# Optimization experiments

Hardware: AMD Instinct MI355X
Metric: run time of the kernel (lower is better)

Reference implementation:

```python
import jax, jax.numpy as jnp
import numpy as np

N, D, H, K, P = 1536, 1024, 16, 64, 8
FREQ_DIM = 14 * 3 * 128  # freq_embedding(pos, 128) flattened


def freq_embedding(t, size):
    # min_freq=0.01, max_freq=2**8 as in the block's call sites
    nf = size // 2
    freqs = (2.0 ** jnp.linspace(np.log2(0.01), np.log2(256.0), nf)).astype(jnp.float32)
    r = t[..., None] * freqs
    return jnp.stack((jnp.sin(r), jnp.cos(r)), axis=-1).reshape(t.shape[0], -1)


def layer_norm(x, eps=1e-5):
    m = jnp.mean(x, -1, keepdims=True)
    v = jnp.var(x, -1, keepdims=True)
    return (x - m) * jax.lax.rsqrt(v + eps)


def cond_norm(x, cond, ws, bs, wb, bb):
    return jax.nn.sigmoid(cond @ ws + bs) * layer_norm(x) + (cond @ wb + bb)


def _unit(v):
    return v * jax.lax.rsqrt(jnp.sum(v * v, -1, keepdims=True) + 1e-8)


def aa_frames(pos):
    # Gram-Schmidt frame from backbone N/CA/C (atom14 slots 0,1,2)
    n, ca, c = pos[:, 0], pos[:, 1], pos[:, 2]
    e1 = _unit(c - ca)
    v2 = n - ca
    e2 = _unit(v2 - jnp.sum(e1 * v2, -1, keepdims=True) * e1)
    e3 = jnp.cross(e1, e2)
    R = jnp.stack([e1, e2, e3], axis=-1)  # [N,3,3]
    return R, ca


def setup_inputs():
    key = jax.random.key(0)
    ks = iter(jax.random.split(key, 64))
    r = lambda *s: jax.random.normal(next(ks), s, jnp.float32)
    w = lambda *s: 0.02 * jax.random.normal(next(ks), s, jnp.float32)
    z = lambda *s: jnp.zeros(s, jnp.float32)
    return dict(
        local=r(N, D), pos=r(N, 14, 3), condition=r(N, D),
        mask=jnp.ones((N,), bool), pair_bias=r(H, N, N),
        w_f1=w(FREQ_DIM, 2 * D), b_f1=z(2 * D), w_f2=w(2 * D, D), b_f2=z(D),
        cn1_ws=w(D, D), cn1_bs=z(D), cn1_wb=w(D, D), cn1_bb=z(D),
        wq=w(D, H * K), wk=w(D, H * K), wv=w(D, H * K),
        wqp=w(D, H * P * 3), wkp=w(D, H * P * 3), wvp=w(D, H * P * 3),
        gamma=z(H), wo=w(H * (K + 4 * P), D), bo=z(D),
        cn2_ws=w(D, D), cn2_bs=z(D), cn2_wb=w(D, D), cn2_bb=z(D),
        wg1=w(D, 2 * D), bg1=z(2 * D), wg2=w(D, 2 * D), bg2=z(2 * D),
        wg3=w(2 * D, D), bg3=z(D),
        cn3_ws=w(D, D), cn3_bs=z(D), cn3_wb=w(D, D), cn3_bb=z(D),
        w_vel=w(D, 14 * 3),
    )


def reference(local, pos, condition, mask, pair_bias,
              w_f1, b_f1, w_f2, b_f2,
              cn1_ws, cn1_bs, cn1_wb, cn1_bb,
              wq, wk, wv, wqp, wkp, wvp, gamma, wo, bo,
              cn2_ws, cn2_bs, cn2_wb, cn2_bb,
              wg1, bg1, wg2, bg2, wg3, bg3,
              cn3_ws, cn3_bs, cn3_wb, cn3_bb, w_vel):
    n = local.shape[0]
    # embed_pred_pos: MLP over freq embedding of coords
    emb = freq_embedding(pos, 128)  # [N, 5376]
    local = local + (jax.nn.silu(emb @ w_f1 + b_f1) @ w_f2 + b_f2)
    # attention branch
    ai = cond_norm(local, condition, cn1_ws, cn1_bs, cn1_wb, cn1_bb)
    R, t = aa_frames(pos)
    q = (ai @ wq).reshape(n, H, K)
    k = (ai @ wk).reshape(n, H, K)
    v = (ai @ wv).reshape(n, H, K)
    to_glob = lambda p: jnp.einsum('nab,nhpb->nhpa', R, p) + t[:, None, None, :]
    qg = to_glob((ai @ wqp).reshape(n, H, P, 3))
    kg = to_glob((ai @ wkp).reshape(n, H, P, 3))
    vg = to_glob((ai @ wvp).reshape(n, H, P, 3))
    qk = jnp.einsum('ihk,jhk->hij', q, k) / np.sqrt(K).astype(np.float32)
    # squared point distances via norm expansion (never materialize [H,N,N,P,3])
    ptdot = jnp.einsum('ihpc,jhpc->hij', qg, kg)
    qn = jnp.sum(qg * qg, axis=(-1, -2)).T  # [H,N]
    kn = jnp.sum(kg * kg, axis=(-1, -2)).T
    dist2 = qn[:, :, None] + kn[None if False else slice(None), None, :] - 2.0 * ptdot
    wc = np.sqrt(2.0 / (9.0 * P)).astype(np.float32)
    logits = qk + pair_bias - 0.5 * wc * jax.nn.softplus(gamma)[:, None, None] * dist2
    logits = jnp.where(mask[None, None, :], logits, -1e9)
    a = jax.nn.softmax(logits, axis=-1)  # [H,N,N]
    o = jnp.einsum('hij,jhk->ihk', a, v).reshape(n, H * K)
    opg = jnp.einsum('hij,jhpc->ihpc', a, vg)
    opl = jnp.einsum('nba,nhpb->nhpa', R, opg - t[:, None, None, :])
    onorm = jnp.sqrt(jnp.sum(opl * opl, -1) + 1e-8).reshape(n, -1)
    upd = jnp.concatenate([o, opl.reshape(n, -1), onorm], axis=-1) @ wo + bo
    local = local + upd
    # gated MLP branch
    x = cond_norm(local, condition, cn2_ws, cn2_bs, cn2_wb, cn2_bb)
    local = local + (jax.nn.silu(x @ wg1 + bg1) * (x @ wg2 + bg2)) @ wg3 + bg3
    # output heads
    ln = cond_norm(local, condition, cn3_ws, cn3_bs, cn3_wb, cn3_bb)
    velocity = (ln @ w_vel).reshape(n, 14, 3)
    return local, velocity
```

## Files before the change

kernel.cpp:

```cpp
#include <hip/hip_runtime.h>
#include <hip/hip_bf16.h>
#include <math.h>

#define NRES 1536
#define NH 16
#define NNF 2359296ull
#define LOG2E 1.44269504f
#define KVS 4
#define LDQ 4224
#define NTPJ 19
#define PROBLK 16914

typedef unsigned short u16;
typedef __attribute__((ext_vector_type(8))) short short8;
typedef __attribute__((ext_vector_type(4))) unsigned short u16x4;
typedef __attribute__((ext_vector_type(4))) float f32x4;

typedef const __attribute__((address_space(1))) void gvoid;
typedef __attribute__((address_space(3))) void lvoid;

__device__ __forceinline__ u16 f2b(float x){
    __hip_bfloat16 h = __float2bfloat16(x);
    return *reinterpret_cast<u16*>(&h);
}
__device__ __forceinline__ float b2f(u16 u){
    unsigned v = ((unsigned)u) << 16;
    return __uint_as_float(v);
}

#define F_BIAS  1
#define F_SILU  2
#define F_RESID 8
#define F_OUTBF 16

template<int TNF>
__global__ __launch_bounds__(256) void gemm_t(
    const u16* __restrict__ A, int lda, size_t zsA,
    const u16* __restrict__ BT, int ldb, size_t zsB,
    float* __restrict__ Cf, u16* __restrict__ Cb, int ldc, size_t zsC,
    const float* __restrict__ bias, size_t zsBias,
    const float* __restrict__ resid, int ldr, size_t zsR,
    int Ncols, int Kd, int flags, int ksl)
{
    constexpr int TN = TNF * 32;
    __shared__ u16 As[2][128 * 64];
    __shared__ u16 Bs[2][TN * 64];

    unsigned gx = gridDim.x, gy = gridDim.y;
    unsigned nb = gx * gy * gridDim.z;
    unsigned bid = (blockIdx.z * gy + blockIdx.y) * gx + blockIdx.x;
    if ((nb & 7u) == 0u) bid = (bid & 7u) * (nb >> 3) + (bid >> 3);
    const int bxi = bid % gx;
    const int byi = (bid / gx) % gy;
    const int bz  = bid / (gx * gy);

    const int tid = threadIdx.x;
    const int l = tid & 63, w = tid >> 6;
    const int bm = byi * 128, bn = bxi * TN;

    A  += zsA * bz;
    BT += zsB * bz;

    const int kbeg = ksl ? bz * ksl : 0;
    const int kend = ksl ? kbeg + ksl : Kd;
    const int nk = (kend - kbeg) >> 6;

    const int arow   = l >> 3;
    const int aslot  = l & 7;
    const int srcslt = aslot ^ arow;

    const u16* aBase[4];
    const u16* bBase[TN / 32];
    #pragma unroll
    for (int t = 0; t < 4; ++t) {
        int ra = bm + (w * 4 + t) * 8 + arow;
        aBase[t] = A + (size_t)ra * lda + srcslt * 8;
    }
    #pragma unroll
    for (int t = 0; t < TN / 32; ++t) {
        int rb = bn + (w * (TN / 32) + t) * 8 + arow;
        if (rb > Ncols - 1) rb = Ncols - 1;
        bBase[t] = BT + (size_t)rb * ldb + srcslt * 8;
    }

    const int wr = w >> 1, wc = w & 1;
    const int fr = l & 15;
    const int fq = l >> 4;

    f32x4 acc[4][TNF];
    #pragma unroll
    for (int i = 0; i < 4; ++i)
        #pragma unroll
        for (int j = 0; j < TNF; ++j) acc[i][j] = (f32x4){0.f, 0.f, 0.f, 0.f};

    auto stage = [&](int buf, int k0) {
        #pragma unroll
        for (int t = 0; t < 4; ++t)
            __builtin_amdgcn_global_load_lds((gvoid*)(aBase[t] + k0),
                (lvoid*)((char*)As[buf] + (w * 4 + t) * 1024), 16, 0, 0);
        #pragma unroll
        for (int t = 0; t < TN / 32; ++t)
            __builtin_amdgcn_global_load_lds((gvoid*)(bBase[t] + k0),
                (lvoid*)((char*)Bs[buf] + (w * (TN / 32) + t) * 1024), 16, 0, 0);
    };

    stage(0, kbeg);
    __syncthreads();
    int cur = 0;

    for (int it = 0; it < nk; ++it) {
        if (it + 1 < nk) stage(cur ^ 1, kbeg + (it + 1) * 64);
        #pragma unroll
        for (int kk = 0; kk < 2; ++kk) {
            const int slotR = ((kk * 4) + fq) ^ (l & 7);
            short8 av[4], bv[TNF];
            #pragma unroll
            for (int m = 0; m < 4; ++m) {
                int r = wr * 64 + m * 16 + fr;
                av[m] = *(const short8*)((const char*)As[cur] + r * 128 + slotR * 16);
            }
            #pragma unroll
            for (int n = 0; n < TNF; ++n) {
                int r = wc * (TNF * 16) + n * 16 + fr;
                bv[n] = *(const short8*)((const char*)Bs[cur] + r * 128 + slotR * 16);
            }
            #pragma unroll
            for (int m = 0; m < 4; ++m)
                #pragma unroll
                for (int n = 0; n < TNF; ++n)
                    acc[m][n] = __builtin_amdgcn_mfma_f32_16x16x32_bf16(av[m], bv[n], acc[m][n], 0, 0, 0);
        }
        __syncthreads();
        cur ^= 1;
    }

    const float* residz = (flags & F_RESID) ? resid + zsR * bz : nullptr;
    const float* biasz  = (flags & F_BIAS)  ? bias + zsBias * bz : nullptr;
    float* cfz = Cf ? Cf + zsC * bz : nullptr;
    u16*   cbz = Cb ? Cb + zsC * bz : nullptr;

    #pragma unroll
    for (int m = 0; m < 4; ++m) {
        #pragma unroll
        for (int n = 0; n < TNF; ++n) {
            int gc = bn + wc * (TNF * 16) + n * 16 + fr;
            if (gc >= Ncols) continue;
            int gr0 = bm + wr * 64 + m * 16 + fq * 4;
            #pragma unroll
            for (int r = 0; r < 4; ++r) {
                int gr = gr0 + r;
                float v = acc[m][n][r];
                if (flags & F_BIAS)  v += biasz[gc];
                if (flags & F_SILU)  v = v / (1.f + expf(-v));
                if (flags & F_RESID) v += residz[(size_t)gr * ldr + gc];
                if (flags & F_OUTBF) cbz[(size_t)gr * ldc + gc] = f2b(v);
                else                 cfz[(size_t)gr * ldc + gc] = v;
            }
        }
    }
}

struct GJob {
    const u16* A;
    const u16* BT;
    u16* C;
    const float* bias;
    int lda, ldb, ldc;
    size_t zsA, zsB, zsC, zsBias;
    int Nc, Kd, ksl, flags;
    unsigned gx, gy, start, nb;
};

__global__ __launch_bounds__(256) void gemm_dual(GJob j0, GJob j1)
{
    __shared__ u16 As[2][128 * 64];
    __shared__ u16 Bs[2][64 * 64];

    GJob J = (blockIdx.x >= j1.start) ? j1 : j0;
    unsigned bid = blockIdx.x - J.start;
    if ((J.nb & 7u) == 0u) bid = (bid & 7u) * (J.nb >> 3) + (bid >> 3);
    const int bxi = bid % J.gx;
    const int byi = (bid / J.gx) % J.gy;
    const int bz  = bid / (J.gx * J.gy);

    const int tid = threadIdx.x;
    const int l = tid & 63, w = tid >> 6;
    const int bm = byi * 128, bn = bxi * 64;

    const u16* A  = J.A + J.zsA * bz;
    const u16* BT = J.BT + J.zsB * bz;

    const int kbeg = J.ksl ? bz * J.ksl : 0;
    const int kend = J.ksl ? kbeg + J.ksl : J.Kd;
    const int nk = (kend - kbeg) >> 6;

    const int arow   = l >> 3;
    const int aslot  = l & 7;
    const int srcslt = aslot ^ arow;

    const u16* aBase[4];
    const u16* bBase[2];
    #pragma unroll
    for (int t = 0; t < 4; ++t) {
        int ra = bm + (w * 4 + t) * 8 + arow;
        aBase[t] = A + (size_t)ra * J.lda + srcslt * 8;
    }
    #pragma unroll
    for (int t = 0; t < 2; ++t) {
        int rb = bn + (w * 2 + t) * 8 + arow;
        if (rb > J.Nc - 1) rb = J.Nc - 1;
        bBase[t] = BT + (size_t)rb * J.ldb + srcslt * 8;
    }

    const int wr = w >> 1, wc = w & 1;
    const int fr = l & 15;
    const int fq = l >> 4;

    f32x4 acc[4][2];
    #pragma unroll
    for (int i = 0; i < 4; ++i)
        #pragma unroll
        for (int j = 0; j < 2; ++j) acc[i][j] = (f32x4){0.f, 0.f, 0.f, 0.f};

    auto stage = [&](int buf, int k0) {
        #pragma unroll
        for (int t = 0; t < 4; ++t)
            __builtin_amdgcn_global_load_lds((gvoid*)(aBase[t] + k0),
                (lvoid*)((char*)As[buf] + (w * 4 + t) * 1024), 16, 0, 0);
        #pragma unroll
        for (int t = 0; t < 2; ++t)
            __builtin_amdgcn_global_load_lds((gvoid*)(bBase[t] + k0),
                (lvoid*)((char*)Bs[buf] + (w * 2 + t) * 1024), 16, 0, 0);
    };

    stage(0, kbeg);
    __syncthreads();
    int cur = 0;

    for (int it = 0; it < nk; ++it) {
        if (it + 1 < nk) stage(cur ^ 1, kbeg + (it + 1) * 64);
        #pragma unroll
        for (int kk = 0; kk < 2; ++kk) {
            const int slotR = ((kk * 4) + fq) ^ (l & 7);
            short8 av[4], bv[2];
            #pragma unroll
            for (int m = 0; m < 4; ++m) {
                int r = wr * 64 + m * 16 + fr;
                av[m] = *(const short8*)((const char*)As[cur] + r * 128 + slotR * 16);
            }
            #pragma unroll
            for (int n = 0; n < 2; ++n) {
                int r = wc * 32 + n * 16 + fr;
                bv[n] = *(const short8*)((const char*)Bs[cur] + r * 128 + slotR * 16);
            }
            #pragma unroll
            for (int m = 0; m < 4; ++m)
                #pragma unroll
                for (int n = 0; n < 2; ++n)
                    acc[m][n] = __builtin_amdgcn_mfma_f32_16x16x32_bf16(av[m], bv[n], acc[m][n], 0, 0, 0);
        }
        __syncthreads();
        cur ^= 1;
    }

    const float* biasz = (J.flags & F_BIAS) ? J.bias + J.zsBias * bz : nullptr;
    u16* cbz = J.C + J.zsC * bz;

    #pragma unroll
    for (int m = 0; m < 4; ++m) {
        #pragma unroll
        for (int n = 0; n < 2; ++n) {
            int gc = bn + wc * 32 + n * 16 + fr;
            if (gc >= J.Nc) continue;
            int gr0 = bm + wr * 64 + m * 16 + fq * 4;
            #pragma unroll
            for (int r = 0; r < 4; ++r) {
                int gr = gr0 + r;
                float v = acc[m][n][r];
                if (J.flags & F_BIAS) v += biasz[gc];
                cbz[(size_t)gr * J.ldc + gc] = f2b(v);
            }
        }
    }
}

__global__ __launch_bounds__(256) void reduce_epi(
    const u16* __restrict__ part, size_t slice, int nsl,
    float* __restrict__ Cf, u16* __restrict__ Cb,
    const float* __restrict__ bias,
    const float* __restrict__ resid, int ldr,
    int M, int Ncols, int flags)
{
    if ((Ncols & 7) == 0) {
        size_t total8 = (size_t)M * Ncols / 8;
        for (size_t i8 = (size_t)blockIdx.x * 256 + threadIdx.x; i8 < total8;
             i8 += (size_t)gridDim.x * 256) {
            size_t i0 = i8 * 8;
            int r = (int)(i0 / (unsigned)Ncols);
            int c0 = (int)(i0 - (size_t)r * Ncols);
            float v[8] = {0,0,0,0,0,0,0,0};
            for (int s = 0; s < nsl; ++s) {
                const u16x4* p = (const u16x4*)(part + (size_t)s * slice + i0);
                u16x4 a = p[0], b = p[1];
                v[0] += b2f(a.x); v[1] += b2f(a.y); v[2] += b2f(a.z); v[3] += b2f(a.w);
                v[4] += b2f(b.x); v[5] += b2f(b.y); v[6] += b2f(b.z); v[7] += b2f(b.w);
            }
            #pragma unroll
            for (int j = 0; j < 8; ++j) {
                if (flags & F_BIAS) v[j] += bias[c0 + j];
                if (flags & F_SILU) v[j] = v[j] / (1.f + expf(-v[j]));
            }
            if (flags & F_RESID) {
                const float4* rp = (const float4*)(resid + (size_t)r * ldr + c0);
                float4 r0 = rp[0], r1 = rp[1];
                v[0] += r0.x; v[1] += r0.y; v[2] += r0.z; v[3] += r0.w;
                v[4] += r1.x; v[5] += r1.y; v[6] += r1.z; v[7] += r1.w;
            }
            if (flags & F_OUTBF) {
                short8 o;
                #pragma unroll
                for (int j = 0; j < 8; ++j) o[j] = (short)f2b(v[j]);
                *(short8*)(Cb + i0) = o;
            } else {
                float4 o0 = {v[0], v[1], v[2], v[3]}, o1 = {v[4], v[5], v[6], v[7]};
                float4* cp = (float4*)(Cf + i0);
                cp[0] = o0; cp[1] = o1;
            }
        }
    } else {
        size_t total = (size_t)M * Ncols;
        for (size_t i = (size_t)blockIdx.x * 256 + threadIdx.x; i < total;
             i += (size_t)gridDim.x * 256) {
            float v = 0.f;
            for (int s = 0; s < nsl; ++s) v += b2f(part[(size_t)s * slice + i]);
            if (flags & F_OUTBF) Cb[i] = f2b(v);
            else                 Cf[i] = v;
        }
    }
}

__global__ __launch_bounds__(256) void reduce_cn(
    const u16* __restrict__ part, size_t slice, int nsl,
    const float* __restrict__ bias, const float* __restrict__ resid,
    float* __restrict__ locOut,
    const u16* __restrict__ cs, const u16* __restrict__ cb,
    u16* __restrict__ normB)
{
    int row = blockIdx.x, tid = threadIdx.x;
    size_t base = (size_t)row * 1024 + tid * 4;
    float v[4];
    {
        float4 rv = *(const float4*)(resid + base);
        v[0] = rv.x; v[1] = rv.y; v[2] = rv.z; v[3] = rv.w;
    }
    for (int s = 0; s < nsl; ++s) {
        u16x4 p = *(const u16x4*)(part + (size_t)s * slice + base);
        v[0] += b2f(p.x); v[1] += b2f(p.y); v[2] += b2f(p.z); v[3] += b2f(p.w);
    }
    {
        float4 bv = *(const float4*)(bias + tid * 4);
        v[0] += bv.x; v[1] += bv.y; v[2] += bv.z; v[3] += bv.w;
    }
    *(float4*)(locOut + base) = (float4){v[0], v[1], v[2], v[3]};

    float s1 = v[0] + v[1] + v[2] + v[3];
    float s2 = v[0]*v[0] + v[1]*v[1] + v[2]*v[2] + v[3]*v[3];
    __shared__ float r1[256], r2[256];
    r1[tid] = s1; r2[tid] = s2;
    __syncthreads();
    for (int st = 128; st > 0; st >>= 1) {
        if (tid < st) { r1[tid] += r1[tid + st]; r2[tid] += r2[tid + st]; }
        __syncthreads();
    }
    float mean = r1[0] * (1.f / 1024.f);
    float var = r2[0] * (1.f / 1024.f) - mean * mean;
    float rs = rsqrtf(var + 1e-5f);
    u16x4 sv = *(const u16x4*)(cs + base);
    u16x4 bv = *(const u16x4*)(cb + base);
    u16x4 o;
    o.x = f2b((1.f / (1.f + expf(-b2f(sv.x)))) * (v[0] - mean) * rs + b2f(bv.x));
    o.y = f2b((1.f / (1.f + expf(-b2f(sv.y)))) * (v[1] - mean) * rs + b2f(bv.y));
    o.z = f2b((1.f / (1.f + expf(-b2f(sv.z)))) * (v[2] - mean) * rs + b2f(bv.z));
    o.w = f2b((1.f / (1.f + expf(-b2f(sv.w)))) * (v[3] - mean) * rs + b2f(bv.w));
    *(u16x4*)(normB + base) = o;
}

__global__ __launch_bounds__(256, 2) void attn_kernel(
    const u16* __restrict__ qe, const u16* __restrict__ ke,
    const u16* __restrict__ vt, const float* __restrict__ pb,
    u16* __restrict__ Opart, float* __restrict__ mlpart)
{
    __shared__ u16 Ks[2][64 * 128];
    __shared__ u16 Vs[2][96 * 64];
    __shared__ u16 Ps[64 * 64];

    unsigned gx = gridDim.x, gy = gridDim.y;
    unsigned nb = gx * gy * gridDim.z;
    unsigned bid = (blockIdx.z * gy + blockIdx.y) * gx + blockIdx.x;
    bid = (bid & 7u) * (nb >> 3) + (bid >> 3);
    const int qx = bid % gx;
    const int h  = (bid / gx) % gy;
    const int z  = bid / (gx * gy);

    const int tid = threadIdx.x;
    const int l = tid & 63, w = tid >> 6;
    const int q0 = qx * 64;
    const int fr = l & 15, fq = l >> 4;

    const u16* keh = ke + (size_t)h * NRES * 128;
    const u16* vth = vt + (size_t)h * 96 * NRES;

    const int kr4 = l >> 4, ks16 = l & 15;
    const int vr8 = l >> 3, vs8 = l & 7;

    short8 qv[4];
    {
        const u16* qrow = qe + ((size_t)h * NRES + (q0 + w * 16 + fr)) * 128 + fq * 8;
        #pragma unroll
        for (int kk = 0; kk < 4; ++kk)
            qv[kk] = *(const short8*)(qrow + kk * 32);
    }

    float m_run[4], l_run[4];
    f32x4 oacc[6];
    #pragma unroll
    for (int r = 0; r < 4; ++r) { m_run[r] = -1e30f; l_run[r] = 0.f; }
    #pragma unroll
    for (int n = 0; n < 6; ++n) oacc[n] = (f32x4){0.f, 0.f, 0.f, 0.f};

    const int NIT = NRES / 64 / KVS;
    const int jbase = z * (NRES / KVS);
    int cur = 0;

    auto stage = [&](int buf, int j0) {
        #pragma unroll
        for (int t = 0; t < 4; ++t) {
            int row = w * 16 + t * 4 + kr4;
            int ss = ks16 ^ (row & 7);
            __builtin_amdgcn_global_load_lds(
                (gvoid*)(keh + (size_t)(j0 + row) * 128 + ss * 8),
                (lvoid*)((char*)Ks[buf] + (w * 16 + t * 4) * 256), 16, 0, 0);
        }
        #pragma unroll
        for (int t = 0; t < 3; ++t) {
            int row = w * 24 + t * 8 + vr8;
            int ss = vs8 ^ (row & 7);
            __builtin_amdgcn_global_load_lds(
                (gvoid*)(vth + (size_t)row * NRES + j0 + ss * 8),
                (lvoid*)((char*)Vs[buf] + (w * 24 + t * 8) * 128), 16, 0, 0);
        }
    };
    const float* pbrow = pb + ((size_t)h * NRES + (q0 + w * 16 + fq * 4)) * NRES + fr;

    f32x4 pbv[4], pbn[4] = {};
    stage(0, jbase);
    #pragma unroll
    for (int n = 0; n < 4; ++n)
        #pragma unroll
        for (int r = 0; r < 4; ++r)
            pbv[n][r] = pbrow[(size_t)r * NRES + jbase + n * 16];
    __syncthreads();

    for (int it = 0; it < NIT; ++it) {
        if (it + 1 < NIT) {
            int j1 = jbase + (it + 1) * 64;
            stage(cur ^ 1, j1);
            #pragma unroll
            for (int n = 0; n < 4; ++n)
                #pragma unroll
                for (int r = 0; r < 4; ++r)
                    pbn[n][r] = pbrow[(size_t)r * NRES + j1 + n * 16];
        }

        f32x4 sacc[4];
        #pragma unroll
        for (int n = 0; n < 4; ++n) sacc[n] = (f32x4){0.f, 0.f, 0.f, 0.f};
        __builtin_amdgcn_s_setprio(1);
        #pragma unroll
        for (int kk = 0; kk < 4; ++kk) {
            #pragma unroll
            for (int n = 0; n < 4; ++n) {
                int row = n * 16 + fr;
                short8 bv = *(const short8*)((const char*)Ks[cur] + row * 256
                                             + (((kk * 4 + fq) ^ (fr & 7)) * 16));
                sacc[n] = __builtin_amdgcn_mfma_f32_16x16x32_bf16(qv[kk], bv, sacc[n], 0, 0, 0);
            }
        }
        __builtin_amdgcn_s_setprio(0);
        #pragma unroll
        for (int n = 0; n < 4; ++n) sacc[n] += pbv[n];

        float alpha[4];
        #pragma unroll
        for (int r = 0; r < 4; ++r) {
            float v = fmaxf(fmaxf(sacc[0][r], sacc[1][r]), fmaxf(sacc[2][r], sacc[3][r]));
            v = fmaxf(v, __shfl_xor(v, 1, 64));
            v = fmaxf(v, __shfl_xor(v, 2, 64));
            v = fmaxf(v, __shfl_xor(v, 4, 64));
            v = fmaxf(v, __shfl_xor(v, 8, 64));
            float mn = fmaxf(m_run[r], v);
            alpha[r] = exp2f((m_run[r] - mn) * LOG2E);
            m_run[r] = mn;
        }

        float psum[4] = {0.f, 0.f, 0.f, 0.f};
        #pragma unroll
        for (int n = 0; n < 4; ++n) {
            int col = n * 16 + fr;
            #pragma unroll
            for (int r = 0; r < 4; ++r) {
                float p = exp2f((sacc[n][r] - m_run[r]) * LOG2E);
                psum[r] += p;
                int rowf = w * 16 + fq * 4 + r;
                int byte = rowf * 128 + (((col >> 3) ^ (rowf & 7)) * 16) + (col & 7) * 2;
                *(u16*)((char*)Ps + byte) = f2b(p);
            }
        }
        #pragma unroll
        for (int r = 0; r < 4; ++r) {
            float v = psum[r];
            v += __shfl_xor(v, 1, 64);
            v += __shfl_xor(v, 2, 64);
            v += __shfl_xor(v, 4, 64);
            v += __shfl_xor(v, 8, 64);
            l_run[r] = l_run[r] * alpha[r] + v;
        }
        #pragma unroll
        for (int n = 0; n < 6; ++n)
            #pragma unroll
            for (int r = 0; r < 4; ++r)
                oacc[n][r] *= alpha[r];

        __builtin_amdgcn_s_setprio(1);
        #pragma unroll
        for (int kk = 0; kk < 2; ++kk) {
            int prow = w * 16 + fr;
            short8 pa = *(const short8*)((const char*)Ps + prow * 128
                                         + (((kk * 4 + fq) ^ (prow & 7)) * 16));
            #pragma unroll
            for (int n = 0; n < 6; ++n) {
                int vrow = n * 16 + fr;
                short8 vv = *(const short8*)((const char*)Vs[cur] + vrow * 128
                                             + (((kk * 4 + fq) ^ (fr & 7)) * 16));
                oacc[n] = __builtin_amdgcn_mfma_f32_16x16x32_bf16(pa, vv, oacc[n], 0, 0, 0);
            }
        }
        __builtin_amdgcn_s_setprio(0);

        __syncthreads();
        cur ^= 1;
        #pragma unroll
        for (int n = 0; n < 4; ++n) pbv[n] = pbn[n];
    }

    u16* Oz = Opart + ((size_t)z * NH + h) * NRES * 96;
    #pragma unroll
    for (int n = 0; n < 6; ++n) {
        int c = n * 16 + fr;
        #pragma unroll
        for (int r = 0; r < 4; ++r) {
            int row = q0 + w * 16 + fq * 4 + r;
            Oz[(size_t)row * 96 + c] = f2b(oacc[n][r]);
        }
    }
    if (fr == 0) {
        float* mlz = mlpart + ((size_t)z * NH + h) * NRES * 2;
        #pragma unroll
        for (int r = 0; r < 4; ++r) {
            int row = q0 + w * 16 + fq * 4 + r;
            mlz[row * 2 + 0] = m_run[r];
            mlz[row * 2 + 1] = l_run[r];
        }
    }
}

__global__ __launch_bounds__(256) void combine_fin(
    const u16* __restrict__ Opart, const float* __restrict__ mlpart,
    const float* __restrict__ Rb, const float* __restrict__ tb,
    u16* __restrict__ featB)
{
    int idx = blockIdx.x * 256 + threadIdx.x;
    if (idx >= NRES * NH) return;
    int n = idx >> 4, h = idx & 15;

    float m[KVS], lv[KVS], wgt[KVS];
    float mm = -1e30f;
    #pragma unroll
    for (int s = 0; s < KVS; ++s) {
        size_t rr = ((size_t)s * NH + h) * NRES + n;
        m[s] = mlpart[rr * 2];
        lv[s] = mlpart[rr * 2 + 1];
        mm = fmaxf(mm, m[s]);
    }
    float ll = 0.f;
    #pragma unroll
    for (int s = 0; s < KVS; ++s) {
        wgt[s] = exp2f((m[s] - mm) * LOG2E);
        ll += lv[s] * wgt[s];
    }
    float inv = 1.f / ll;
    const u16* op[KVS];
    #pragma unroll
    for (int s = 0; s < KVS; ++s)
        op[s] = Opart + (((size_t)s * NH + h) * NRES + n) * 96;

    u16* fb = featB + (size_t)n * 1536;
    #pragma unroll
    for (int k = 0; k < 64; ++k) {
        float v = 0.f;
        #pragma unroll
        for (int s = 0; s < KVS; ++s) v += b2f(op[s][k]) * wgt[s];
        fb[h * 64 + k] = f2b(v * inv);
    }

    float R[9];
    #pragma unroll
    for (int a = 0; a < 9; ++a) R[a] = Rb[(size_t)n * 9 + a];
    float t0 = tb[(size_t)n * 3 + 0], t1 = tb[(size_t)n * 3 + 1], t2 = tb[(size_t)n * 3 + 2];
    #pragma unroll
    for (int p = 0; p < 8; ++p) {
        float d[3];
        #pragma unroll
        for (int dd = 0; dd < 3; ++dd) {
            int c = 64 + p * 3 + dd;
            float v = 0.f;
            #pragma unroll
            for (int s = 0; s < KVS; ++s) v += b2f(op[s][c]) * wgt[s];
            d[dd] = v * inv;
        }
        float x = d[0] - t0, y = d[1] - t1, z = d[2] - t2;
        float a0 = R[0] * x + R[3] * y + R[6] * z;
        float a1 = R[1] * x + R[4] * y + R[7] * z;
        float a2 = R[2] * x + R[5] * y + R[8] * z;
        fb[1024 + h * 24 + p * 3 + 0] = f2b(a0);
        fb[1024 + h * 24 + p * 3 + 1] = f2b(a1);
        fb[1024 + h * 24 + p * 3 + 2] = f2b(a2);
        fb[1408 + h * 8 + p] = f2b(sqrtf(a0 * a0 + a1 * a1 + a2 * a2 + 1e-8f));
    }
}

struct TpMega {
    const float* src[NTPJ];
    u16* dst[NTPJ];
    int ldi[NTPJ], ldo[NTPJ], K[NTPJ], N[NTPJ];
    int bx[NTPJ], start[NTPJ];
};

__global__ __launch_bounds__(256) void prep_kernel(
    const float* __restrict__ pos, const float* __restrict__ cond,
    const float* __restrict__ cn1_bs, const float* __restrict__ cn1_bb,
    const float* __restrict__ cn2_bs, const float* __restrict__ cn2_bb,
    const float* __restrict__ cn3_bs, const float* __restrict__ cn3_bb,
    const float* __restrict__ bg1, const float* __restrict__ bg2,
    float* __restrict__ Rb, float* __restrict__ tb,
    u16* __restrict__ emb, u16* __restrict__ condB,
    float* __restrict__ bias2, float* __restrict__ biasg,
    TpMega J)
{
    __shared__ float t[32][33];
    int b = blockIdx.x, tid = threadIdx.x;
    if (b >= PROBLK) {
        int tb2 = b - PROBLK;
        int j = NTPJ - 1;
        while (J.start[j] > tb2) --j;
        int lb = tb2 - J.start[j];
        int bxn = J.bx[j];
        int n0 = (lb % bxn) * 32;
        int k0 = (lb / bxn) * 32;
        const float* in = J.src[j];
        u16* out = J.dst[j];
        int ldi = J.ldi[j], ldo = J.ldo[j], Kk = J.K[j], Nn = J.N[j];
        int tx = tid & 31, ty = tid >> 5;
        #pragma unroll
        for (int jj = 0; jj < 4; ++jj) {
            int k = k0 + ty + jj * 8;
            if (k < Kk && n0 + tx < Nn) t[ty + jj * 8][tx] = in[(size_t)k * ldi + n0 + tx];
        }
        __syncthreads();
        #pragma unroll
        for (int jj = 0; jj < 4; ++jj) {
            int n = n0 + ty + jj * 8;
            int k = k0 + tx;
            if (n < Nn && k < Kk) out[(size_t)n * ldo + k] = f2b(t[tx][ty + jj * 8]);
        }
        return;
    }
    if (b < 16128) {
        int idx = b * 256 + tid;
        int f = idx & 63;
        int rest = idx >> 6;
        int coord = rest % 42;
        int n = rest / 42;
        float tt = pos[(size_t)n * 42 + coord];
        const double l0 = -6.643856189774724;
        const double step = 14.643856189774724 / 63.0;
        float freq = exp2f((float)(l0 + f * step));
        float r = tt * freq;
        size_t o = (size_t)n * 5376 + (size_t)coord * 128 + 2 * f;
        emb[o]     = f2b(sinf(r));
        emb[o + 1] = f2b(cosf(r));
    } else if (b < 16896) {
        int i = (b - 16128) * 256 + tid;
        size_t i0 = (size_t)i * 8;
        const float4* p = (const float4*)(cond + i0);
        float4 a = p[0], bb = p[1];
        short8 o;
        o[0]=(short)f2b(a.x); o[1]=(short)f2b(a.y); o[2]=(short)f2b(a.z); o[3]=(short)f2b(a.w);
        o[4]=(short)f2b(bb.x); o[5]=(short)f2b(bb.y); o[6]=(short)f2b(bb.z); o[7]=(short)f2b(bb.w);
        *(short8*)(condB + i0) = o;
    } else if (b < 16902) {
        int n = (b - 16896) * 256 + tid;
        if (n >= NRES) return;
        const float* p = pos + (size_t)n * 42;
        float nx = p[0], ny = p[1], nz = p[2];
        float cax = p[3], cay = p[4], caz = p[5];
        float cx = p[6], cy = p[7], cz = p[8];
        float v1x = cx - cax, v1y = cy - cay, v1z = cz - caz;
        float i1 = rsqrtf(v1x * v1x + v1y * v1y + v1z * v1z + 1e-8f);
        float e1x = v1x * i1, e1y = v1y * i1, e1z = v1z * i1;
        float v2x = nx - cax, v2y = ny - cay, v2z = nz - caz;
        float d = e1x * v2x + e1y * v2y + e1z * v2z;
        float wx = v2x - d * e1x, wy = v2y - d * e1y, wz = v2z - d * e1z;
        float i2 = rsqrtf(wx * wx + wy * wy + wz * wz + 1e-8f);
        float e2x = wx * i2, e2y = wy * i2, e2z = wz * i2;
        float e3x = e1y * e2z - e1z * e2y;
        float e3y = e1z * e2x - e1x * e2z;
        float e3z = e1x * e2y - e1y * e2x;
        float* R = Rb + (size_t)n * 9;
        R[0] = e1x; R[1] = e2x; R[2] = e3x;
        R[3] = e1y; R[4] = e2y; R[5] = e3y;
        R[6] = e1z; R[7] = e2z; R[8] = e3z;
        tb[(size_t)n * 3 + 0] = cax;
        tb[(size_t)n * 3 + 1] = cay;
        tb[(size_t)n * 3 + 2] = caz;
    } else if (b < 16906) {
        int i = (b - 16902) * 256 + tid;
        if (i >= 1024) return;
        bias2[i] = cn1_bs[i]; bias2[1024 + i] = cn1_bb[i]; bias2[2048 + i] = cn2_bs[i];
        bias2[3072 + i] = cn2_bb[i]; bias2[4096 + i] = cn3_bs[i]; bias2[5120 + i] = cn3_bb[i];
    } else {
        int i = (b - 16906) * 256 + tid;
        if (i >= 2048) return;
        biasg[i] = bg1[i]; biasg[2048 + i] = bg2[i];
    }
}

__global__ __launch_bounds__(256) void pack_all(
    const u16* __restrict__ qkc,
    const float* __restrict__ Rb, const float* __restrict__ tb,
    const float* __restrict__ gamma,
    u16* __restrict__ qe, u16* __restrict__ ke, u16* __restrict__ vt)
{
    int b = blockIdx.x;
    if (b < 1536) {
        int idx = b * 256 + threadIdx.x;
        int g = idx & 15;
        int t = idx >> 4;
        int n = t % NRES;
        int h = t / NRES;
        size_t o = ((size_t)h * NRES + n) * 128 + g * 8;
        if (g < 8) {
            short8 q8 = *(const short8*)(qkc + (size_t)n * LDQ + h * 64 + g * 8);
            short8 k8 = *(const short8*)(qkc + (size_t)n * LDQ + 1024 + h * 64 + g * 8);
            short8 oq;
            #pragma unroll
            for (int j = 0; j < 8; ++j) oq[j] = (short)f2b(0.125f * b2f((u16)q8[j]));
            *(short8*)(qe + o) = oq;
            *(short8*)(ke + o) = k8;
        } else if (g >= 11) {
            short8 zz = {};
            *(short8*)(qe + o) = zz;
            *(short8*)(ke + o) = zz;
        }
        return;
    }
    if (b < 1632) {
        int idx = (b - 1536) * 256 + threadIdx.x;
        if (idx >= NRES * NH) return;
        int n = idx >> 4, h = idx & 15;
        float R[9];
        #pragma unroll
        for (int a = 0; a < 9; ++a) R[a] = Rb[(size_t)n * 9 + a];
        float t0 = tb[(size_t)n * 3 + 0], t1 = tb[(size_t)n * 3 + 1], t2 = tb[(size_t)n * 3 + 2];
        float g = gamma[h];
        float sp = (g > 20.f) ? g : log1pf(expf(g));
        float ch = 0.5f * (1.f / 6.f) * sp;

        u16* qeh = qe + ((size_t)h * NRES + n) * 128;
        u16* keh = ke + ((size_t)h * NRES + n) * 128;
        const u16* qp = qkc + (size_t)n * LDQ + 3072 + h * 24;
        const u16* kp = qkc + (size_t)n * LDQ + 3456 + h * 24;
        float kn = 0.f;
        #pragma unroll
        for (int p = 0; p < 8; ++p) {
            {
                float x = b2f(qp[p*3]), y = b2f(qp[p*3+1]), z = b2f(qp[p*3+2]);
                float g0 = R[0] * x + R[1] * y + R[2] * z + t0;
                float g1 = R[3] * x + R[4] * y + R[5] * z + t1;
                float g2 = R[6] * x + R[7] * y + R[8] * z + t2;
                qeh[64 + p * 3 + 0] = f2b(2.f * ch * g0);
                qeh[64 + p * 3 + 1] = f2b(2.f * ch * g1);
                qeh[64 + p * 3 + 2] = f2b(2.f * ch * g2);
            }
            {
                float x = b2f(kp[p*3]), y = b2f(kp[p*3+1]), z = b2f(kp[p*3+2]);
                float g0 = R[0] * x + R[1] * y + R[2] * z + t0;
                float g1 = R[3] * x + R[4] * y + R[5] * z + t1;
                float g2 = R[6] * x + R[7] * y + R[8] * z + t2;
                keh[64 + p * 3 + 0] = f2b(g0);
                keh[64 + p * 3 + 1] = f2b(g1);
                keh[64 + p * 3 + 2] = f2b(g2);
                kn += g0 * g0 + g1 * g1 + g2 * g2;
            }
        }
        qeh[88] = f2b(1.0f);
        keh[88] = f2b(-ch * kn);
        return;
    }
    __shared__ float t[32][33];
    int lb = b - 1632;
    int h = lb / 144;
    int rem = lb - h * 144;
    int grp = rem / 48;
    int n0 = (rem - grp * 48) * 32;
    int tx = threadIdx.x & 31, ty = threadIdx.x >> 5;
    #pragma unroll
    for (int j = 0; j < 4; ++j) {
        int n = n0 + ty + j * 8;
        int c = grp * 32 + tx;
        float v = 0.f;
        if (c < 64) {
            v = b2f(qkc[(size_t)n * LDQ + 2048 + h * 64 + c]);
        } else if (c < 88) {
            int pc = c - 64;
            int p = pc / 3, a = pc - p * 3;
            const u16* vp = qkc + (size_t)n * LDQ + 3840 + h * 24 + p * 3;
            float x = b2f(vp[0]), y = b2f(vp[1]), z = b2f(vp[2]);
            v = Rb[(size_t)n * 9 + 3 * a + 0] * x + Rb[(size_t)n * 9 + 3 * a + 1] * y
              + Rb[(size_t)n * 9 + 3 * a + 2] * z + tb[(size_t)n * 3 + a];
        }
        t[ty + j * 8][tx] = v;
    }
    __syncthreads();
    #pragma unroll
    for (int j = 0; j < 4; ++j) {
        int r = grp * 32 + ty + j * 8;
        vt[((size_t)h * 96 + r) * NRES + n0 + tx] = f2b(t[tx][ty + j * 8]);
    }
}

__global__ __launch_bounds__(256) void glu_kernel(const u16* __restrict__ g12, u16* __restrict__ gm)
{
    int i = blockIdx.x * 256 + threadIdx.x;
    if (i >= NRES * 2048 / 8) return;
    size_t i0 = (size_t)i * 8;
    short8 a8 = *(const short8*)(g12 + i0);
    short8 b8 = *(const short8*)(g12 + (size_t)NRES * 2048 + i0);
    short8 o;
    #pragma unroll
    for (int j = 0; j < 8; ++j) {
        float a = b2f((u16)a8[j]);
        float b = b2f((u16)b8[j]);
        float s = a / (1.f + expf(-a));
        o[j] = (short)f2b(s * b);
    }
    *(short8*)(gm + i0) = o;
}

extern "C" void kernel_launch(void* const* d_in, const int* in_sizes, int n_in,
                              void* d_out, int out_size, void* d_ws, size_t ws_size,
                              hipStream_t stream)
{
    const float* local_in = (const float*)d_in[0];
    const float* pos      = (const float*)d_in[1];
    const float* cond     = (const float*)d_in[2];
    const float* pb       = (const float*)d_in[4];
    const float* w_f1     = (const float*)d_in[5];
    const float* b_f1     = (const float*)d_in[6];
    const float* w_f2     = (const float*)d_in[7];
    const float* b_f2     = (const float*)d_in[8];
    const float* cn1_ws   = (const float*)d_in[9];
    const float* cn1_bs   = (const float*)d_in[10];
    const float* cn1_wb   = (const float*)d_in[11];
    const float* cn1_bb   = (const float*)d_in[12];
    const float* wq       = (const float*)d_in[13];
    const float* wk       = (const float*)d_in[14];
    const float* wv       = (const float*)d_in[15];
    const float* wqp      = (const float*)d_in[16];
    const float* wkp      = (const float*)d_in[17];
    const float* wvp      = (const float*)d_in[18];
    const float* gamma    = (const float*)d_in[19];
    const float* wo       = (const float*)d_in[20];
    const float* bo       = (const float*)d_in[21];
    const float* cn2_ws   = (const float*)d_in[22];
    const float* cn2_bs   = (const float*)d_in[23];
    const float* cn2_wb   = (const float*)d_in[24];
    const float* cn2_bb   = (const float*)d_in[25];
    const float* wg1      = (const float*)d_in[26];
    const float* bg1      = (const float*)d_in[27];
    const float* wg2      = (const float*)d_in[28];
    const float* bg2      = (const float*)d_in[29];
    const float* wg3      = (const float*)d_in[30];
    const float* bg3      = (const float*)d_in[31];
    const float* cn3_ws   = (const float*)d_in[32];
    const float* cn3_bs   = (const float*)d_in[33];
    const float* cn3_wb   = (const float*)d_in[34];
    const float* cn3_bb   = (const float*)d_in[35];
    const float* w_vel    = (const float*)d_in[36];

    float* out = (float*)d_out;
    float* ws  = (float*)d_ws;

    size_t off = 0;
    auto alloc = [&](size_t nf) -> float* { float* p = ws + off; off += (nf + 7) & ~7ull; return p; };

    const size_t NN1 = (size_t)NRES * 1024;
    float* Rb    = alloc(NRES * 9);
    float* tb    = alloc(NRES * 3);
    float* loc   = alloc(NN1);
    u16*   cs6b  = (u16*)alloc(6 * NN1 / 2);
    u16*   condB = (u16*)alloc(NN1 / 2);
    u16*   normB = (u16*)alloc(NN1 / 2);
    float* bias2 = alloc(6 * 1024);
    float* biasg = alloc(2 * 2048);
    u16*   qkcB  = (u16*)alloc((size_t)NRES * LDQ / 2);
    u16*   qeB   = (u16*)alloc((size_t)NH * NRES * 128 / 2);
    u16*   keB   = (u16*)alloc((size_t)NH * NRES * 128 / 2);
    u16*   vTB   = (u16*)alloc((size_t)NH * 96 * NRES / 2);
    u16*   featB = (u16*)alloc((size_t)NRES * 1536 / 2);
    u16*   g1sB  = (u16*)alloc((size_t)NRES * 2048 / 2);
    u16*   gmB   = (u16*)alloc((size_t)NRES * 2048 / 2);
    u16*   cnT9  = (u16*)alloc((size_t)9 * 1024 * 1024 / 2);
    u16*   ptsT  = (u16*)alloc((size_t)3 * 384 * 1024 / 2);
    u16*   wgT   = (u16*)alloc((size_t)2 * 2048 * 1024 / 2);
    u16*   wf1T  = (u16*)alloc((size_t)2048 * 5376 / 2);
    u16*   wf2T  = (u16*)alloc((size_t)1024 * 2048 / 2);
    u16*   woT   = (u16*)alloc((size_t)1024 * 1536 / 2);
    u16*   wg3T  = (u16*)alloc((size_t)1024 * 2048 / 2);
    u16*   wvT   = (u16*)alloc((size_t)42 * 1024 / 2 + 8);
    u16*   embB  = (u16*)alloc((size_t)NRES * 5376 / 2);
    u16*   hidB  = (u16*)alloc((size_t)NRES * 2048 / 2);
    u16*   pscr  = (u16*)alloc((size_t)2 * NRES * 2048 * 4 / 2);
    u16*   Opart = (u16*)alloc((size_t)KVS * NH * NRES * 96 / 2);
    float* mlprt = alloc((size_t)KVS * NH * NRES * 2);

    const float* nilf = nullptr;

    auto gemm = [&](int tnf, const u16* A, int lda, size_t zsA,
                    const u16* BT, int ldb, size_t zsB,
                    float* Cf, u16* Cb2, int ldc, size_t zsC,
                    const float* bias, size_t zsBias,
                    const float* resid, int ldr, size_t zsR,
                    int Nc, int Kd, int flags, int gz, int ksl) {
        int tn = tnf * 32;
        dim3 grid((Nc + tn - 1) / tn, NRES / 128, gz);
        if (tnf == 4)
            hipLaunchKernelGGL(gemm_t<4>, grid, dim3(256), 0, stream,
                               A, lda, zsA, BT, ldb, zsB, Cf, Cb2, ldc, zsC,
                               bias, zsBias, resid, ldr, zsR, Nc, Kd, flags, ksl);
        else
            hipLaunchKernelGGL(gemm_t<2>, grid, dim3(256), 0, stream,
                               A, lda, zsA, BT, ldb, zsB, Cf, Cb2, ldc, zsC,
                               bias, zsBias, resid, ldr, zsR, Nc, Kd, flags, ksl);
    };
    auto red = [&](const u16* part, size_t slice, int nsl, float* Cf, u16* Cb2,
                   const float* bias, const float* resid, int ldr, int Nc, int flags) {
        hipLaunchKernelGGL(reduce_epi, dim3(1024), dim3(256), 0, stream,
                           part, slice, nsl, Cf, Cb2, bias, resid, ldr, NRES, Nc, flags);
    };
    auto redcn = [&](const u16* part, size_t slice, int nsl,
                     const float* bias, const float* resid, float* locOut, int cnIdx) {
        hipLaunchKernelGGL(reduce_cn, dim3(NRES), dim3(256), 0, stream,
                           part, slice, nsl, bias, resid, locOut,
                           cs6b + (size_t)(2 * cnIdx) * NN1,
                           cs6b + (size_t)(2 * cnIdx + 1) * NN1, normB);
    };

    {
        TpMega J;
        int jn = 0, start = 0;
        auto addJob = [&](const float* src, u16* dst, int ldi, int ldo, int K, int N) {
            J.src[jn] = src; J.dst[jn] = dst;
            J.ldi[jn] = ldi; J.ldo[jn] = ldo; J.K[jn] = K; J.N[jn] = N;
            int bx = (N + 31) / 32, by = (K + 31) / 32;
            J.bx[jn] = bx; J.start[jn] = start;
            start += bx * by;
            ++jn;
        };
        const float* cn6[6] = {cn1_ws, cn1_wb, cn2_ws, cn2_wb, cn3_ws, cn3_wb};
        for (int i = 0; i < 6; ++i)
            addJob(cn6[i], cnT9 + (size_t)i * 1024 * 1024, 1024, 1024, 1024, 1024);
        addJob(wq, cnT9 + (size_t)6 * 1024 * 1024, 1024, 1024, 1024, 1024);
        addJob(wk, cnT9 + (size_t)7 * 1024 * 1024, 1024, 1024, 1024, 1024);
        addJob(wv, cnT9 + (size_t)8 * 1024 * 1024, 1024, 1024, 1024, 1024);
        addJob(wqp, ptsT,                        384, 1024, 1024, 384);
        addJob(wkp, ptsT + (size_t)384 * 1024,   384, 1024, 1024, 384);
        addJob(wvp, ptsT + (size_t)2 * 384 * 1024, 384, 1024, 1024, 384);
        addJob(wg1, wgT,                        2048, 1024, 1024, 2048);
        addJob(wg2, wgT + (size_t)2048 * 1024,  2048, 1024, 1024, 2048);
        addJob(w_f1, wf1T, 2048, 5376, 5376, 2048);
        addJob(w_f2, wf2T, 1024, 2048, 2048, 1024);
        addJob(wo,   woT,  1024, 1536, 1536, 1024);
        addJob(wg3,  wg3T, 1024, 2048, 2048, 1024);
        addJob(w_vel, wvT,   42, 1024, 1024, 42);
        hipLaunchKernelGGL(prep_kernel, dim3(PROBLK + start), dim3(256), 0, stream,
                           pos, cond, cn1_bs, cn1_bb, cn2_bs, cn2_bb, cn3_bs, cn3_bb,
                           bg1, bg2, Rb, tb, embB, condB, bias2, biasg, J);
    }

    {
        GJob jc, je;
        jc.A = condB; jc.BT = cnT9; jc.C = cs6b; jc.bias = bias2;
        jc.lda = 1024; jc.ldb = 1024; jc.ldc = 1024;
        jc.zsA = 0; jc.zsB = (size_t)1024 * 1024; jc.zsC = NN1; jc.zsBias = 1024;
        jc.Nc = 1024; jc.Kd = 1024; jc.ksl = 0; jc.flags = F_BIAS;
        jc.gx = 16; jc.gy = 12; jc.start = 0; jc.nb = 16 * 12 * 6;
        je.A = embB; je.BT = wf1T; je.C = pscr; je.bias = nullptr;
        je.lda = 5376; je.ldb = 5376; je.ldc = 2048;
        je.zsA = 0; je.zsB = 0; je.zsC = (size_t)NRES * 2048; je.zsBias = 0;
        je.Nc = 2048; je.Kd = 5376; je.ksl = 1344; je.flags = 0;
        je.gx = 32; je.gy = 12; je.start = jc.nb; je.nb = 32 * 12 * 4;
        hipLaunchKernelGGL(gemm_dual, dim3(jc.nb + je.nb), dim3(256), 0, stream, jc, je);
    }
    red(pscr, (size_t)NRES * 2048, 4, nullptr, hidB, b_f1, nilf, 0,
        2048, F_BIAS | F_SILU | F_OUTBF);
    gemm(2, hidB, 2048, 0, wf2T, 2048, 0, nullptr, pscr, 1024, NN1,
         nilf, 0, nilf, 0, 0, 1024, 2048, F_OUTBF, 4, 512);
    redcn(pscr, NN1, 4, b_f2, local_in, loc, 0);

    gemm(2, normB, 1024, 0, cnT9 + (size_t)6 * 1024 * 1024, 1024, 0,
         nullptr, qkcB, LDQ, 0, nilf, 0, nilf, 0, 0, LDQ, 1024, F_OUTBF, 1, 0);

    hipLaunchKernelGGL(pack_all, dim3(1632 + 2304), dim3(256), 0, stream,
                       qkcB, Rb, tb, gamma, qeB, keB, vTB);

    hipLaunchKernelGGL(attn_kernel, dim3(NRES / 64, NH, KVS), dim3(256), 0, stream,
                       qeB, keB, vTB, pb, Opart, mlprt);
    hipLaunchKernelGGL(combine_fin, dim3(96), dim3(256), 0, stream,
                       Opart, mlprt, Rb, tb, featB);

    gemm(2, featB, 1536, 0, woT, 1536, 0, nullptr, pscr, 1024, NN1,
         nilf, 0, nilf, 0, 0, 1024, 1536, F_OUTBF, 4, 384);
    redcn(pscr, NN1, 4, bo, loc, loc, 1);

    gemm(2, normB, 1024, 0, wgT, 1024, (size_t)2048 * 1024, nullptr, g1sB, 2048, (size_t)NRES * 2048,
         biasg, 2048, nilf, 0, 0, 2048, 1024, F_BIAS | F_OUTBF, 2, 0);
    u16* gmO = embB;
    hipLaunchKernelGGL(glu_kernel, dim3((NRES * 2048 / 8 + 255) / 256), dim3(256), 0, stream, g1sB, gmO);
    gemm(2, gmO, 2048, 0, wg3T, 2048, 0, nullptr, pscr, 1024, NN1,
         nilf, 0, nilf, 0, 0, 1024, 2048, F_OUTBF, 4, 512);
    redcn(pscr, NN1, 4, bg3, loc, out, 2);

    gemm(2, normB, 1024, 0, wvT, 1024, 0, nullptr, pscr, 42, (size_t)NRES * 42,
         nilf, 0, nilf, 0, 0, 42, 1024, F_OUTBF, 8, 128);
    red(pscr, (size_t)NRES * 42, 8, out + (size_t)NRES * 1024, nullptr,
        nilf, nilf, 0, 42, 0);
}
```

Baseline: 433.9 us.

## Fuse velocity head into final cond-norm reduce and parallelize combine_fin

The velocity projection (normalized activations times w_vel) is computed inside the last reduce_cn kernel through per-thread partial dot products and a shared-memory reduction. This removes the separate weight transpose job, the split-K GEMM and the reduce launch. combine_fin is also spread across more threads, one thread per output chunk instead of one per (residue, head). The trade-offs are a large per-thread register array and 44KB of shared memory in the fused kernel, plus redundant softmax-weight recomputation in each combine thread.

```diff
diff --git a/kernel.cpp b/kernel.cpp
--- a/kernel.cpp
+++ b/kernel.cpp
@@ -8,7 +8,7 @@
 #define LOG2E 1.44269504f
 #define KVS 4
 #define LDQ 4224
-#define NTPJ 19
+#define NTPJ 18
 #define PROBLK 16914
 
 typedef unsigned short u16;
@@ -339,12 +339,14 @@
     }
 }
 
+template<int DOVEL>
 __global__ __launch_bounds__(256) void reduce_cn(
     const u16* __restrict__ part, size_t slice, int nsl,
     const float* __restrict__ bias, const float* __restrict__ resid,
     float* __restrict__ locOut,
     const u16* __restrict__ cs, const u16* __restrict__ cb,
-    u16* __restrict__ normB)
+    u16* __restrict__ normB,
+    const float* __restrict__ wvel, float* __restrict__ velOut)
 {
     int row = blockIdx.x, tid = threadIdx.x;
     size_t base = (size_t)row * 1024 + tid * 4;
@@ -383,6 +385,28 @@
     o.z = f2b((1.f / (1.f + expf(-b2f(sv.z)))) * (v[2] - mean) * rs + b2f(bv.z));
     o.w = f2b((1.f / (1.f + expf(-b2f(sv.w)))) * (v[3] - mean) * rs + b2f(bv.w));
     *(u16x4*)(normB + base) = o;
+
+    if (DOVEL) {
+        __shared__ float pv[DOVEL ? 256 * 43 : 1];
+        float nv[4] = {b2f(o.x), b2f(o.y), b2f(o.z), b2f(o.w)};
+        float part42[42];
+        #pragma unroll
+        for (int c = 0; c < 42; ++c) part42[c] = 0.f;
+        #pragma unroll
+        for (int j = 0; j < 4; ++j) {
+            const float* wv = wvel + (size_t)(tid * 4 + j) * 42;
+            #pragma unroll
+            for (int c = 0; c < 42; ++c) part42[c] += nv[j] * wv[c];
+        }
+        #pragma unroll
+        for (int c = 0; c < 42; ++c) pv[tid * 43 + c] = part42[c];
+        __syncthreads();
+        if (tid < 42) {
+            float s = 0.f;
+            for (int t2 = 0; t2 < 256; ++t2) s += pv[t2 * 43 + tid];
+            velOut[(size_t)row * 42 + tid] = s;
+        }
+    }
 }
 
 __global__ __launch_bounds__(256, 2) void attn_kernel(
@@ -580,8 +604,11 @@
     u16* __restrict__ featB)
 {
     int idx = blockIdx.x * 256 + threadIdx.x;
-    if (idx >= NRES * NH) return;
-    int n = idx >> 4, h = idx & 15;
+    if (idx >= NRES * NH * 32) return;
+    int j = idx & 31;
+    if (j >= 24) return;
+    int t = idx >> 5;
+    int n = t >> 4, h = t & 15;
 
     float m[KVS], lv[KVS], wgt[KVS];
     float mm = -1e30f;
@@ -605,38 +632,40 @@
         op[s] = Opart + (((size_t)s * NH + h) * NRES + n) * 96;
 
     u16* fb = featB + (size_t)n * 1536;
-    #pragma unroll
-    for (int k = 0; k < 64; ++k) {
+    if (j < 16) {
+        int c0 = j * 4;
+        #pragma unroll
+        for (int q = 0; q < 4; ++q) {
+            int c = c0 + q;
+            float v = 0.f;
+            #pragma unroll
+            for (int s = 0; s < KVS; ++s) v += b2f(op[s][c]) * wgt[s];
+            fb[h * 64 + c] = f2b(v * inv);
+        }
+        return;
+    }
+    int p = j - 16;
+    float d[3];
+    #pragma unroll
+    for (int dd = 0; dd < 3; ++dd) {
+        int c = 64 + p * 3 + dd;
         float v = 0.f;
         #pragma unroll
-        for (int s = 0; s < KVS; ++s) v += b2f(op[s][k]) * wgt[s];
-        fb[h * 64 + k] = f2b(v * inv);
-    }
-
+        for (int s = 0; s < KVS; ++s) v += b2f(op[s][c]) * wgt[s];
+        d[dd] = v * inv;
+    }
     float R[9];
     #pragma unroll
     for (int a = 0; a < 9; ++a) R[a] = Rb[(size_t)n * 9 + a];
     float t0 = tb[(size_t)n * 3 + 0], t1 = tb[(size_t)n * 3 + 1], t2 = tb[(size_t)n * 3 + 2];
-    #pragma unroll
-    for (int p = 0; p < 8; ++p) {
-        float d[3];
-        #pragma unroll
-        for (int dd = 0; dd < 3; ++dd) {
-            int c = 64 + p * 3 + dd;
-            float v = 0.f;
-            #pragma unroll
-            for (int s = 0; s < KVS; ++s) v += b2f(op[s][c]) * wgt[s];
-            d[dd] = v * inv;
-        }
-        float x = d[0] - t0, y = d[1] - t1, z = d[2] - t2;
-        float a0 = R[0] * x + R[3] * y + R[6] * z;
-        float a1 = R[1] * x + R[4] * y + R[7] * z;
-        float a2 = R[2] * x + R[5] * y + R[8] * z;
-        fb[1024 + h * 24 + p * 3 + 0] = f2b(a0);
-        fb[1024 + h * 24 + p * 3 + 1] = f2b(a1);
-        fb[1024 + h * 24 + p * 3 + 2] = f2b(a2);
-        fb[1408 + h * 8 + p] = f2b(sqrtf(a0 * a0 + a1 * a1 + a2 * a2 + 1e-8f));
-    }
+    float x = d[0] - t0, y = d[1] - t1, z = d[2] - t2;
+    float a0 = R[0] * x + R[3] * y + R[6] * z;
+    float a1 = R[1] * x + R[4] * y + R[7] * z;
+    float a2 = R[2] * x + R[5] * y + R[8] * z;
+    fb[1024 + h * 24 + p * 3 + 0] = f2b(a0);
+    fb[1024 + h * 24 + p * 3 + 1] = f2b(a1);
+    fb[1024 + h * 24 + p * 3 + 2] = f2b(a2);
+    fb[1408 + h * 8 + p] = f2b(sqrtf(a0 * a0 + a1 * a1 + a2 * a2 + 1e-8f));
 }
 
 struct TpMega {
@@ -937,7 +966,6 @@
     u16*   wf2T  = (u16*)alloc((size_t)1024 * 2048 / 2);
     u16*   woT   = (u16*)alloc((size_t)1024 * 1536 / 2);
     u16*   wg3T  = (u16*)alloc((size_t)1024 * 2048 / 2);
-    u16*   wvT   = (u16*)alloc((size_t)42 * 1024 / 2 + 8);
     u16*   embB  = (u16*)alloc((size_t)NRES * 5376 / 2);
     u16*   hidB  = (u16*)alloc((size_t)NRES * 2048 / 2);
     u16*   pscr  = (u16*)alloc((size_t)2 * NRES * 2048 * 4 / 2);
@@ -969,11 +997,19 @@
                            part, slice, nsl, Cf, Cb2, bias, resid, ldr, NRES, Nc, flags);
     };
     auto redcn = [&](const u16* part, size_t slice, int nsl,
-                     const float* bias, const float* resid, float* locOut, int cnIdx) {
-        hipLaunchKernelGGL(reduce_cn, dim3(NRES), dim3(256), 0, stream,
-                           part, slice, nsl, bias, resid, locOut,
-                           cs6b + (size_t)(2 * cnIdx) * NN1,
-                           cs6b + (size_t)(2 * cnIdx + 1) * NN1, normB);
+                     const float* bias, const float* resid, float* locOut, int cnIdx,
+                     const float* wvel, float* velOut) {
+        if (wvel)
+            hipLaunchKernelGGL(reduce_cn<1>, dim3(NRES), dim3(256), 0, stream,
+                               part, slice, nsl, bias, resid, locOut,
+                               cs6b + (size_t)(2 * cnIdx) * NN1,
+                               cs6b + (size_t)(2 * cnIdx + 1) * NN1, normB, wvel, velOut);
+        else
+            hipLaunchKernelGGL(reduce_cn<0>, dim3(NRES), dim3(256), 0, stream,
+                               part, slice, nsl, bias, resid, locOut,
+                               cs6b + (size_t)(2 * cnIdx) * NN1,
+                               cs6b + (size_t)(2 * cnIdx + 1) * NN1, normB,
+                               (const float*)nullptr, (float*)nullptr);
     };
 
     {
@@ -1002,7 +1038,6 @@
         addJob(w_f2, wf2T, 1024, 2048, 2048, 1024);
         addJob(wo,   woT,  1024, 1536, 1536, 1024);
         addJob(wg3,  wg3T, 1024, 2048, 2048, 1024);
-        addJob(w_vel, wvT,   42, 1024, 1024, 42);
         hipLaunchKernelGGL(prep_kernel, dim3(PROBLK + start), dim3(256), 0, stream,
                            pos, cond, cn1_bs, cn1_bb, cn2_bs, cn2_bb, cn3_bs, cn3_bb,
                            bg1, bg2, Rb, tb, embB, condB, bias2, biasg, J);
@@ -1026,7 +1061,7 @@
         2048, F_BIAS | F_SILU | F_OUTBF);
     gemm(2, hidB, 2048, 0, wf2T, 2048, 0, nullptr, pscr, 1024, NN1,
          nilf, 0, nilf, 0, 0, 1024, 2048, F_OUTBF, 4, 512);
-    redcn(pscr, NN1, 4, b_f2, local_in, loc, 0);
+    redcn(pscr, NN1, 4, b_f2, local_in, loc, 0, nilf, nullptr);
 
     gemm(2, normB, 1024, 0, cnT9 + (size_t)6 * 1024 * 1024, 1024, 0,
          nullptr, qkcB, LDQ, 0, nilf, 0, nilf, 0, 0, LDQ, 1024, F_OUTBF, 1, 0);
@@ -1036,12 +1071,12 @@
 
     hipLaunchKernelGGL(attn_kernel, dim3(NRES / 64, NH, KVS), dim3(256), 0, stream,
                        qeB, keB, vTB, pb, Opart, mlprt);
-    hipLaunchKernelGGL(combine_fin, dim3(96), dim3(256), 0, stream,
+    hipLaunchKernelGGL(combine_fin, dim3((NRES * NH * 32) / 256), dim3(256), 0, stream,
                        Opart, mlprt, Rb, tb, featB);
 
     gemm(2, featB, 1536, 0, woT, 1536, 0, nullptr, pscr, 1024, NN1,
          nilf, 0, nilf, 0, 0, 1024, 1536, F_OUTBF, 4, 384);
-    redcn(pscr, NN1, 4, bo, loc, loc, 1);
+    redcn(pscr, NN1, 4, bo, loc, loc, 1, nilf, nullptr);
 
     gemm(2, normB, 1024, 0, wgT, 1024, (size_t)2048 * 1024, nullptr, g1sB, 2048, (size_t)NRES * 2048,
          biasg, 2048, nilf, 0, 0, 2048, 1024, F_BIAS | F_OUTBF, 2, 0);
@@ -1049,10 +1084,5 @@
     hipLaunchKernelGGL(glu_kernel, dim3((NRES * 2048 / 8 + 255) / 256), dim3(256), 0, stream, g1sB, gmO);
     gemm(2, gmO, 2048, 0, wg3T, 2048, 0, nullptr, pscr, 1024, NN1,
          nilf, 0, nilf, 0, 0, 1024, 2048, F_OUTBF, 4, 512);
-    redcn(pscr, NN1, 4, bg3, loc, out, 2);
-
-    gemm(2, normB, 1024, 0, wvT, 1024, 0, nullptr, pscr, 42, (size_t)NRES * 42,
-         nilf, 0, nilf, 0, 0, 42, 1024, F_OUTBF, 8, 128);
-    red(pscr, (size_t)NRES * 42, 8, out + (size_t)NRES * 1024, nullptr,
-        nilf, nilf, 0, 42, 0);
-}
+    redcn(pscr, NN1, 4, bg3, loc, out, 2, w_vel, out + NN1);
+}
```

Result: no change. 440.7 us (+1.6%).
